# Performance work log

Hardware: AMD Instinct MI355X
Metric: run time of the kernel (lower is better)

The kernel has to match this reference:

```python
import jax, jax.numpy as jnp
import numpy as np

B, H, N, D = 2, 12, 2048, 64
M = int(D * np.log(D))          # 266 performer random features
E3 = 3 * D                      # performer value hidden size = head_dim*3
DH2 = 2 * D                     # predictor enc hidden = head_dim*2
T = 128                         # attention_predictor_length
CHUNK = 128                     # chunk size for causal linear attention scan
KERNEL_EPS = 1e-3               # performer generalized-kernel epsilon
D_EPS = 1e-6                    # denominator epsilon (added to k_cumsum)
LN_EPS = 1e-5


def setup_inputs() -> dict:
    key = jax.random.key(0)
    ks = jax.random.split(key, 10)
    return {
        "q": jax.random.normal(ks[0], (B, H, N, D), jnp.float32),
        "k": jax.random.normal(ks[1], (B, H, N, D), jnp.float32),
        "v3": jax.random.normal(ks[2], (B, H, N, E3), jnp.float32),
        "proj": jax.random.normal(ks[3], (M, D), jnp.float32),
        "enc_w": jax.random.normal(ks[4], (E3, DH2), jnp.float32) * 0.05,
        "enc_b": jnp.zeros((DH2,), jnp.float32),
        "ln_g": jnp.ones((DH2,), jnp.float32),
        "ln_b": jnp.zeros((DH2,), jnp.float32),
        "dec_w": jax.random.normal(ks[5], (DH2, T), jnp.float32) * 0.05,
        "dec_b": jnp.zeros((T,), jnp.float32),
    }


def _generalized_features(x, proj):
    # performer generalized attention kernel: relu((x / d^0.25) @ proj^T) + eps
    dn = 1.0 / (x.shape[-1] ** 0.25)
    xp = jnp.einsum("bhnd,md->bhnm", x * dn, proj)
    return jax.nn.relu(xp) + KERNEL_EPS


def _causal_linear_attention(qf, kf, v):
    # qf, kf: [B,H,N,M]; v: [B,H,N,E]. Chunked recurrent form of
    # out[n] = (qf[n] . cumsum(kf)[n])^-1 * qf[n] @ cumsum(kf[m] v[m]^T)[n]
    nE = v.shape[-1]
    nc = N // CHUNK
    qc = qf.reshape(B, H, nc, CHUNK, M).transpose(2, 0, 1, 3, 4)
    kc = kf.reshape(B, H, nc, CHUNK, M).transpose(2, 0, 1, 3, 4)
    vc = v.reshape(B, H, nc, CHUNK, nE).transpose(2, 0, 1, 3, 4)
    mask = jnp.tril(jnp.ones((CHUNK, CHUNK), qf.dtype))

    def step(carry, inp):
        ksum, S = carry                      # [B,H,M], [B,H,M,E]
        q_c, k_c, v_c = inp                  # [B,H,C,M], [B,H,C,M], [B,H,C,E]
        qk = jnp.einsum("bhim,bhjm->bhij", q_c, k_c) * mask  # causal within chunk
        # denominator: qf[n] . (k_cumsum[n] + eps)
        d = (jnp.einsum("bhcm,bhm->bhc", q_c, ksum)
             + qk.sum(-1)
             + D_EPS * q_c.sum(-1))
        out = (jnp.einsum("bhcm,bhme->bhce", q_c, S)
               + jnp.einsum("bhij,bhje->bhie", qk, v_c)) / d[..., None]
        ksum = ksum + k_c.sum(axis=2)
        S = S + jnp.einsum("bhcm,bhce->bhme", k_c, v_c)
        return (ksum, S), out

    init = (jnp.zeros((B, H, M), qf.dtype), jnp.zeros((B, H, M, nE), qf.dtype))
    _, outs = jax.lax.scan(step, init, (qc, kc, vc))
    return outs.transpose(1, 2, 0, 3, 4).reshape(B, H, N, nE)


def reference(q, k, v3, proj, enc_w, enc_b, ln_g, ln_b, dec_w, dec_b):
    qf = _generalized_features(q, proj)
    kf = _generalized_features(k, proj)
    ctx = _causal_linear_attention(qf, kf, v3)            # [B,H,N,3D]
    # attention predictor: Linear -> LayerNorm -> GELU -> Linear -> softmax
    h = jnp.einsum("bhne,ec->bhnc", ctx, enc_w) + enc_b    # [B,H,N,2D]
    mu = h.mean(-1, keepdims=True)
    var = ((h - mu) ** 2).mean(-1, keepdims=True)
    h = (h - mu) * jax.lax.rsqrt(var + LN_EPS) * ln_g + ln_b
    h = jax.nn.gelu(h, approximate=False)
    scores = jnp.einsum("bhnc,ct->bhnt", h, dec_w) + dec_b  # [B,H,N,T]
    est_probs = jax.nn.softmax(scores, axis=-1)
    return ctx, est_probs
```

## Files before the change

### kernel.cpp

```cpp
#include <hip/hip_runtime.h>
#include <hip/hip_bf16.h>
#include <math.h>

constexpr int Bn = 2, Hn = 12, BHn = 24;
constexpr int Nn = 2048, Dn = 64;
constexpr int Mn = 266, MPn = 272;
constexpr int E3n = 192, DHn = 128, Tn = 128;
constexpr int Cn = 128, NCn = 16;

#define DNRM 0.35355339059327373f
#define KEPS 1e-3f
#define DEPS 1e-6f
#define LNEPS 1e-5f

static const size_t OFF_QF   = 0;
static const size_t OFF_KF   = 26738688;
static const size_t OFF_QK   = 53477376;
static const size_t OFF_D    = 66060288;
static const size_t OFF_KPRE = 66256896;
static const size_t OFF_S    = 66674688;
static const size_t OFF_WT   = OFF_KF;
static const size_t WS_NEED  = 106782720;

using bf16x8 = __attribute__((ext_vector_type(8))) short;
using f32x4  = __attribute__((ext_vector_type(4))) float;

__device__ inline float u2f(unsigned int u) {
  union { float f; unsigned int i; } c; c.i = u << 16; return c.f;
}
__device__ inline unsigned short f2u(float x) {
  __hip_bfloat16 h = __float2bfloat16(x);
  unsigned short u; __builtin_memcpy(&u, &h, 2); return u;
}
__device__ inline void unpack8(uint4 v, float* a) {
  a[0] = u2f(v.x & 0xffffu); a[1] = u2f(v.x >> 16);
  a[2] = u2f(v.y & 0xffffu); a[3] = u2f(v.y >> 16);
  a[4] = u2f(v.z & 0xffffu); a[5] = u2f(v.z >> 16);
  a[6] = u2f(v.w & 0xffffu); a[7] = u2f(v.w >> 16);
}
__device__ inline ushort4 f4tobf(float4 v) {
  ushort4 o;
  o.x = f2u(v.x); o.y = f2u(v.y); o.z = f2u(v.z); o.w = f2u(v.w);
  return o;
}

__global__ __launch_bounds__(256) void k_features_mfma(
    const float* __restrict__ q, const float* __restrict__ k,
    const float* __restrict__ proj,
    unsigned short* __restrict__ qf, unsigned short* __restrict__ kf) {
  __shared__ unsigned short at[64][40];
  __shared__ unsigned short bt[272][40];
  const float* x = (blockIdx.y == 0) ? q : k;
  unsigned short* outp = (blockIdx.y == 0) ? qf : kf;
  int tid = threadIdx.x;
  int w = tid >> 6, l = tid & 63;
  int l16 = l & 15, lg = l >> 4;
  int r0 = blockIdx.x * 64;

  f32x4 acc[17] = {};
  for (int kt = 0; kt < 2; ++kt) {
    int k0 = kt * 32;
    __syncthreads();
    #pragma unroll
    for (int p = 0; p < 2; ++p) {
      int idx = tid + p * 256;
      int row = idx >> 3, kq = idx & 7;
      float4 v = *(const float4*)(x + (size_t)(r0 + row) * Dn + k0 + kq * 4);
      *(ushort4*)&at[row][kq * 4] = f4tobf(v);
    }
    for (int idx = tid; idx < 2176; idx += 256) {
      int mq = idx >> 3, kq = idx & 7;
      float4 v = make_float4(0.f, 0.f, 0.f, 0.f);
      if (mq < Mn) v = *(const float4*)(proj + (size_t)mq * Dn + k0 + kq * 4);
      *(ushort4*)&bt[mq][kq * 4] = f4tobf(v);
    }
    __syncthreads();
    bf16x8 a = *(const bf16x8*)((const char*)&at[0][0] + (w*16 + l16) * 80 + lg * 16);
    #pragma unroll
    for (int ct = 0; ct < 17; ++ct) {
      bf16x8 b = *(const bf16x8*)((const char*)&bt[0][0] + (ct*16 + l16) * 80 + lg * 16);
      acc[ct] = __builtin_amdgcn_mfma_f32_16x16x32_bf16(a, b, acc[ct], 0, 0, 0);
    }
  }
  #pragma unroll
  for (int ct = 0; ct < 17; ++ct)
    #pragma unroll
    for (int reg = 0; reg < 4; ++reg) {
      int row = r0 + w*16 + lg*4 + reg;
      int m = ct*16 + l16;
      float val = 0.f;
      if (m < Mn) val = fmaxf(acc[ct][reg] * DNRM, 0.f) + KEPS;
      outp[(size_t)row * MPn + m] = f2u(val);
    }
}

__global__ __launch_bounds__(256) void k_kprefix(float* __restrict__ kpre) {
  int bh = blockIdx.x; int tid = threadIdx.x;
  for (int m = tid; m < MPn; m += 256) {
    float v[NCn];
    #pragma unroll
    for (int c = 0; c < NCn; ++c) v[c] = kpre[((size_t)bh * NCn + c) * MPn + m];
    float acc = 0.f;
    #pragma unroll
    for (int c = 0; c < NCn; ++c) {
      kpre[((size_t)bh * NCn + c) * MPn + m] = acc;
      acc += v[c];
    }
  }
}

__global__ __launch_bounds__(256) void k_qk_mfma(
    const unsigned short* __restrict__ qf,
    const unsigned short* __restrict__ kf,
    const float* __restrict__ kpre,
    unsigned short* __restrict__ qkout,
    float* __restrict__ dden) {
  __shared__ unsigned short at[128][40];
  __shared__ unsigned short ktl[128][40];
  __shared__ float kp[MPn];
  __shared__ float rs_lds[128];
  int blk = blockIdx.x;
  int bh = blk >> 4, c = blk & 15;
  int tid = threadIdx.x;
  int w = tid >> 6, l = tid & 63;
  int l16 = l & 15, lg = l >> 4;
  size_t qbase = ((size_t)bh * Nn + (size_t)c * Cn) * MPn;
  size_t rbase = (size_t)bh * Nn + (size_t)c * Cn;
  for (int m = tid; m < MPn; m += 256) kp[m] = kpre[((size_t)bh * NCn + c) * MPn + m];

  f32x4 acc[2][8] = {};
  for (int kt = 0; kt < 9; ++kt) {
    int mt = kt * 32;
    __syncthreads();
    #pragma unroll
    for (int p = 0; p < 2; ++p) {
      int idx = tid * 8 + p * 2048;
      int r = idx >> 5, kk = idx & 31;
      uint4 va = make_uint4(0u,0u,0u,0u), vk = make_uint4(0u,0u,0u,0u);
      if (mt + kk < MPn) {
        va = *(const uint4*)(qf + qbase + (size_t)r * MPn + mt + kk);
        vk = *(const uint4*)(kf + qbase + (size_t)r * MPn + mt + kk);
      }
      *(uint4*)((char*)&at[0][0] + r * 80 + kk * 2) = va;
      *(uint4*)((char*)&ktl[0][0] + r * 80 + kk * 2) = vk;
    }
    __syncthreads();
    bf16x8 a0 = *(const bf16x8*)((const char*)&at[0][0] + (w*32 + l16) * 80 + lg * 16);
    bf16x8 a1 = *(const bf16x8*)((const char*)&at[0][0] + (w*32 + 16 + l16) * 80 + lg * 16);
    #pragma unroll
    for (int ct = 0; ct < 8; ++ct) {
      bf16x8 b = *(const bf16x8*)((const char*)&ktl[0][0] + (ct*16 + l16) * 80 + lg * 16);
      acc[0][ct] = __builtin_amdgcn_mfma_f32_16x16x32_bf16(a0, b, acc[0][ct], 0, 0, 0);
      acc[1][ct] = __builtin_amdgcn_mfma_f32_16x16x32_bf16(a1, b, acc[1][ct], 0, 0, 0);
    }
  }
  size_t qkbase = (size_t)blk * (Cn * Cn);
  float rs[2][4] = {};
  #pragma unroll
  for (int rt = 0; rt < 2; ++rt)
    #pragma unroll
    for (int ct = 0; ct < 8; ++ct)
      #pragma unroll
      for (int reg = 0; reg < 4; ++reg) {
        int row = w*32 + rt*16 + lg*4 + reg;
        int col = ct*16 + l16;
        float v = (col <= row) ? acc[rt][ct][reg] : 0.f;
        qkout[qkbase + (size_t)row * Cn + col] = f2u(v);
        rs[rt][reg] += v;
      }
  #pragma unroll
  for (int rt = 0; rt < 2; ++rt)
    #pragma unroll
    for (int reg = 0; reg < 4; ++reg) {
      float s = rs[rt][reg];
      s += __shfl_xor(s, 1); s += __shfl_xor(s, 2);
      s += __shfl_xor(s, 4); s += __shfl_xor(s, 8);
      rs[rt][reg] = s;
    }
  if (l16 == 0) {
    #pragma unroll
    for (int rt = 0; rt < 2; ++rt)
      #pragma unroll
      for (int reg = 0; reg < 4; ++reg)
        rs_lds[w*32 + rt*16 + lg*4 + reg] = rs[rt][reg];
  }
  __syncthreads();
  if (tid < 128) {
    float dot = 0.f, qs = 0.f;
    const unsigned short* qrow = qf + qbase + (size_t)tid * MPn;
    for (int m = 0; m < MPn; m += 8) {
      uint4 v = *(const uint4*)(qrow + m);
      float a[8]; unpack8(v, a);
      #pragma unroll
      for (int t = 0; t < 8; ++t) { dot += a[t] * kp[m + t]; qs += a[t]; }
    }
    dden[rbase + tid] = rs_lds[tid] + dot + DEPS * qs;
  }
}

__global__ __launch_bounds__(768) void k_schunk_mfma(
    const unsigned short* __restrict__ kf,
    const float* __restrict__ v3,
    unsigned short* __restrict__ ST,
    float* __restrict__ kpre) {
  __shared__ unsigned short at[192][40];
  __shared__ unsigned short bt[272][36];
  int blk = blockIdx.x;
  int bh = blk >> 4, c = blk & 15;
  int tid = threadIdx.x;
  int w = tid >> 6, l = tid & 63;
  int l16 = l & 15, lg = l >> 4;
  size_t vbase = ((size_t)bh * Nn + (size_t)c * Cn) * E3n;
  size_t kbase = ((size_t)bh * Nn + (size_t)c * Cn) * MPn;

  f32x4 acc[17] = {};
  float ks = 0.f;
  for (int kt = 0; kt < 4; ++kt) {
    int jt = kt * 32;
    __syncthreads();
    #pragma unroll
    for (int p = 0; p < 2; ++p) {
      int idx = tid + p * 768;
      int j = idx & 31, eq = idx >> 5;
      float4 v = *(const float4*)(v3 + vbase + (size_t)(jt + j) * E3n + eq * 4);
      at[eq*4+0][j] = f2u(v.x); at[eq*4+1][j] = f2u(v.y);
      at[eq*4+2][j] = f2u(v.z); at[eq*4+3][j] = f2u(v.w);
    }
    for (int idx = tid; idx < 1088; idx += 768) {
      int j = idx & 31, mq = idx >> 5;
      uint4 v = *(const uint4*)(kf + kbase + (size_t)(jt + j) * MPn + mq * 8);
      unsigned short tmp[8]; __builtin_memcpy(tmp, &v, 16);
      #pragma unroll
      for (int t = 0; t < 8; ++t) bt[mq*8+t][j] = tmp[t];
    }
    __syncthreads();
    bf16x8 a = *(const bf16x8*)((const char*)&at[0][0] + (w*16 + l16) * 80 + lg * 16);
    #pragma unroll
    for (int ct = 0; ct < 17; ++ct) {
      bf16x8 b = *(const bf16x8*)((const char*)&bt[0][0] + (ct*16 + l16) * 72 + lg * 16);
      acc[ct] = __builtin_amdgcn_mfma_f32_16x16x32_bf16(a, b, acc[ct], 0, 0, 0);
    }
    if (tid < MPn) {
      #pragma unroll
      for (int jq = 0; jq < 4; ++jq) {
        uint4 v = *(const uint4*)((const char*)&bt[0][0] + tid * 72 + jq * 16);
        float a8[8]; unpack8(v, a8);
        #pragma unroll
        for (int t = 0; t < 8; ++t) ks += a8[t];
      }
    }
  }
  size_t stbase = (size_t)blk * MPn * E3n;
  #pragma unroll
  for (int ct = 0; ct < 17; ++ct)
    #pragma unroll
    for (int reg = 0; reg < 4; ++reg) {
      int e_loc = w*16 + lg*4 + reg;
      ST[stbase + (size_t)e_loc * MPn + ct*16 + l16] = f2u(acc[ct][reg]);
    }
  if (tid < MPn)
    kpre[((size_t)bh * NCn + c) * MPn + tid] = ks;
}

__global__ __launch_bounds__(256) void k_wt(const float* __restrict__ enc_w,
    const float* __restrict__ dec_w, unsigned short* __restrict__ ewt,
    unsigned short* __restrict__ dwt) {
  int i = blockIdx.x * 256 + threadIdx.x;
  if (i < 128 * 192) {
    int n = i / 192, e = i - n * 192;
    ewt[i] = f2u(enc_w[(size_t)e * DHn + n]);
  } else {
    int j = i - 128 * 192;
    int t = j >> 7, c = j & 127;
    dwt[(size_t)t * DHn + c] = f2u(dec_w[(size_t)c * Tn + t]);
  }
}

__global__ __launch_bounds__(256) void k_sprefix(unsigned short* __restrict__ S) {
  int bh = blockIdx.x / 51, sub = blockIdx.x % 51;
  int idx4 = sub * 256 + threadIdx.x;
  size_t off = (size_t)idx4 * 4;
  ushort4 v[NCn];
  #pragma unroll
  for (int c = 0; c < NCn; ++c)
    v[c] = *(const ushort4*)(S + ((size_t)(bh * NCn + c)) * MPn * E3n + off);
  float a0 = 0.f, a1 = 0.f, a2 = 0.f, a3 = 0.f;
  #pragma unroll
  for (int c = 0; c < NCn; ++c) {
    ushort4 o;
    unsigned short* op = (unsigned short*)&o;
    op[0] = f2u(a0); op[1] = f2u(a1); op[2] = f2u(a2); op[3] = f2u(a3);
    *(ushort4*)(S + ((size_t)(bh * NCn + c)) * MPn * E3n + off) = o;
    a0 += u2f(v[c].x); a1 += u2f(v[c].y); a2 += u2f(v[c].z); a3 += u2f(v[c].w);
  }
}

__global__ __launch_bounds__(768) void k_ctx_mfma(
    const unsigned short* __restrict__ qf,
    const unsigned short* __restrict__ qkm,
    const unsigned short* __restrict__ ST,
    const float* __restrict__ v3,
    const float* __restrict__ dden,
    float* __restrict__ ctx) {
  __shared__ unsigned short at[128][40];
  __shared__ unsigned short bt[192][40];
  __shared__ float dd[128];
  int blk = blockIdx.x;
  int bh = blk >> 4, c = blk & 15;
  int tid = threadIdx.x;
  int w = tid >> 6, l = tid & 63;
  int l16 = l & 15, lg = l >> 4;
  int wr = w & 3, we = w >> 2;
  size_t qbase = ((size_t)bh * Nn + (size_t)c * Cn) * MPn;
  size_t sbase = (size_t)blk * MPn * E3n;
  size_t rbase = (size_t)bh * Nn + (size_t)c * Cn;
  if (tid < 128) dd[tid] = dden[rbase + tid];

  f32x4 acc[2][4] = {};
  for (int kt = 0; kt < 9; ++kt) {
    int mt = kt * 32;
    __syncthreads();
    if (tid < 512) {
      int r = tid >> 2, kk = (tid & 3) * 8;
      uint4 v = make_uint4(0u,0u,0u,0u);
      if (mt + kk < MPn) v = *(const uint4*)(qf + qbase + (size_t)r * MPn + mt + kk);
      *(uint4*)((char*)&at[0][0] + r * 80 + kk * 2) = v;
    }
    {
      int r = tid >> 2, kk = (tid & 3) * 8;
      uint4 v = make_uint4(0u,0u,0u,0u);
      if (mt + kk < MPn) v = *(const uint4*)(ST + sbase + (size_t)r * MPn + mt + kk);
      *(uint4*)((char*)&bt[0][0] + r * 80 + kk * 2) = v;
    }
    __syncthreads();
    bf16x8 a0 = *(const bf16x8*)((const char*)&at[0][0] + (wr*32 + l16) * 80 + lg * 16);
    bf16x8 a1 = *(const bf16x8*)((const char*)&at[0][0] + (wr*32 + 16 + l16) * 80 + lg * 16);
    #pragma unroll
    for (int ct = 0; ct < 4; ++ct) {
      bf16x8 b = *(const bf16x8*)((const char*)&bt[0][0] + (we*64 + ct*16 + l16) * 80 + lg * 16);
      acc[0][ct] = __builtin_amdgcn_mfma_f32_16x16x32_bf16(a0, b, acc[0][ct], 0, 0, 0);
      acc[1][ct] = __builtin_amdgcn_mfma_f32_16x16x32_bf16(a1, b, acc[1][ct], 0, 0, 0);
    }
  }
  size_t kkbase = (size_t)blk * (Cn * Cn);
  size_t vb3 = ((size_t)bh * Nn + (size_t)c * Cn) * E3n;
  for (int kt = 0; kt < 4; ++kt) {
    int jt = kt * 32;
    __syncthreads();
    if (tid < 512) {
      int r = tid >> 2, kk = (tid & 3) * 8;
      uint4 v = *(const uint4*)(qkm + kkbase + (size_t)r * Cn + jt + kk);
      *(uint4*)((char*)&at[0][0] + r * 80 + kk * 2) = v;
    }
    #pragma unroll
    for (int p = 0; p < 2; ++p) {
      int idx = tid + p * 768;
      int j = idx & 31, eq = idx >> 5;
      float4 v = *(const float4*)(v3 + vb3 + (size_t)(jt + j) * E3n + eq * 4);
      bt[eq*4+0][j] = f2u(v.x); bt[eq*4+1][j] = f2u(v.y);
      bt[eq*4+2][j] = f2u(v.z); bt[eq*4+3][j] = f2u(v.w);
    }
    __syncthreads();
    bf16x8 a0 = *(const bf16x8*)((const char*)&at[0][0] + (wr*32 + l16) * 80 + lg * 16);
    bf16x8 a1 = *(const bf16x8*)((const char*)&at[0][0] + (wr*32 + 16 + l16) * 80 + lg * 16);
    #pragma unroll
    for (int ct = 0; ct < 4; ++ct) {
      bf16x8 b = *(const bf16x8*)((const char*)&bt[0][0] + (we*64 + ct*16 + l16) * 80 + lg * 16);
      acc[0][ct] = __builtin_amdgcn_mfma_f32_16x16x32_bf16(a0, b, acc[0][ct], 0, 0, 0);
      acc[1][ct] = __builtin_amdgcn_mfma_f32_16x16x32_bf16(a1, b, acc[1][ct], 0, 0, 0);
    }
  }
  #pragma unroll
  for (int rt = 0; rt < 2; ++rt)
    #pragma unroll
    for (int ct = 0; ct < 4; ++ct)
      #pragma unroll
      for (int reg = 0; reg < 4; ++reg) {
        int row = wr*32 + rt*16 + lg*4 + reg;
        float inv = 1.f / dd[row];
        ctx[(rbase + row) * (size_t)E3n + we*64 + ct*16 + l16] = acc[rt][ct][reg] * inv;
      }
}

__global__ __launch_bounds__(256) void k_pred_fused(
    const float* __restrict__ ctx,
    const unsigned short* __restrict__ ewt,
    const unsigned short* __restrict__ dwt,
    const float* __restrict__ enc_b, const float* __restrict__ ln_g,
    const float* __restrict__ ln_b, const float* __restrict__ dec_b,
    float* __restrict__ probs) {
  __shared__ unsigned short at[128][40];
  __shared__ unsigned short bt[128][40];
  __shared__ unsigned short ht[128][200];
  int tid = threadIdx.x;
  int w = tid >> 6, l = tid & 63;
  int l16 = l & 15, lg = l >> 4;
  size_t r0 = (size_t)blockIdx.x * 128;

  float ebv[8], ggv[8], llv[8], dbv[8];
  #pragma unroll
  for (int ct = 0; ct < 8; ++ct) {
    ebv[ct] = enc_b[ct*16 + l16];
    ggv[ct] = ln_g[ct*16 + l16];
    llv[ct] = ln_b[ct*16 + l16];
    dbv[ct] = dec_b[ct*16 + l16];
  }

  f32x4 acc1[2][8] = {};
  for (int kt = 0; kt < 6; ++kt) {
    int k0 = kt * 32;
    __syncthreads();
    #pragma unroll
    for (int p = 0; p < 4; ++p) {
      int idx = tid + p * 256;
      int row = idx >> 3, kq = idx & 7;
      float4 v = *(const float4*)(ctx + (r0 + row) * E3n + k0 + kq * 4);
      *(ushort4*)&at[row][kq * 4] = f4tobf(v);
    }
    #pragma unroll
    for (int p = 0; p < 2; ++p) {
      int idx = tid + p * 256;
      int n = idx >> 2, kq = idx & 3;
      *(uint4*)&bt[n][kq * 8] = *(const uint4*)(ewt + (size_t)n * E3n + k0 + kq * 8);
    }
    __syncthreads();
    bf16x8 a0 = *(const bf16x8*)((const char*)&at[0][0] + (w*32 + l16) * 80 + lg * 16);
    bf16x8 a1 = *(const bf16x8*)((const char*)&at[0][0] + (w*32 + 16 + l16) * 80 + lg * 16);
    #pragma unroll
    for (int ct = 0; ct < 8; ++ct) {
      bf16x8 b = *(const bf16x8*)((const char*)&bt[0][0] + (ct*16 + l16) * 80 + lg * 16);
      acc1[0][ct] = __builtin_amdgcn_mfma_f32_16x16x32_bf16(a0, b, acc1[0][ct], 0, 0, 0);
      acc1[1][ct] = __builtin_amdgcn_mfma_f32_16x16x32_bf16(a1, b, acc1[1][ct], 0, 0, 0);
    }
  }
  #pragma unroll
  for (int rt = 0; rt < 2; ++rt) {
    #pragma unroll
    for (int reg = 0; reg < 4; ++reg) {
      float hv[8];
      float s = 0.f, s2 = 0.f;
      #pragma unroll
      for (int ct = 0; ct < 8; ++ct) {
        float v = acc1[rt][ct][reg] + ebv[ct];
        hv[ct] = v; s += v; s2 += v * v;
      }
      #pragma unroll
      for (int m = 1; m < 16; m <<= 1) { s += __shfl_xor(s, m); s2 += __shfl_xor(s2, m); }
      float mu = s * (1.f / 128.f);
      float var = s2 * (1.f / 128.f) - mu * mu;
      float rsq = rsqrtf(var + LNEPS);
      int row = w*32 + rt*16 + lg*4 + reg;
      #pragma unroll
      for (int ct = 0; ct < 8; ++ct) {
        float v = (hv[ct] - mu) * rsq * ggv[ct] + llv[ct];
        v = 0.5f * v * (1.f + erff(v * 0.70710678118654752f));
        ht[row][ct*16 + l16] = f2u(v);
      }
    }
  }
  f32x4 acc2[2][8] = {};
  for (int kt = 0; kt < 4; ++kt) {
    int c0 = kt * 32;
    __syncthreads();
    #pragma unroll
    for (int p = 0; p < 2; ++p) {
      int idx = tid + p * 256;
      int t = idx >> 2, kq = idx & 3;
      *(uint4*)&bt[t][kq * 8] = *(const uint4*)(dwt + (size_t)t * DHn + c0 + kq * 8);
    }
    __syncthreads();
    bf16x8 a0 = *(const bf16x8*)&ht[w*32 + l16][c0 + lg*8];
    bf16x8 a1 = *(const bf16x8*)&ht[w*32 + 16 + l16][c0 + lg*8];
    #pragma unroll
    for (int ct = 0; ct < 8; ++ct) {
      bf16x8 b = *(const bf16x8*)((const char*)&bt[0][0] + (ct*16 + l16) * 80 + lg * 16);
      acc2[0][ct] = __builtin_amdgcn_mfma_f32_16x16x32_bf16(a0, b, acc2[0][ct], 0, 0, 0);
      acc2[1][ct] = __builtin_amdgcn_mfma_f32_16x16x32_bf16(a1, b, acc2[1][ct], 0, 0, 0);
    }
  }
  #pragma unroll
  for (int rt = 0; rt < 2; ++rt) {
    #pragma unroll
    for (int reg = 0; reg < 4; ++reg) {
      float sv[8];
      float m = -1e30f;
      #pragma unroll
      for (int ct = 0; ct < 8; ++ct) {
        sv[ct] = acc2[rt][ct][reg] + dbv[ct];
        m = fmaxf(m, sv[ct]);
      }
      #pragma unroll
      for (int mm = 1; mm < 16; mm <<= 1) m = fmaxf(m, __shfl_xor(m, mm));
      float s = 0.f;
      #pragma unroll
      for (int ct = 0; ct < 8; ++ct) { sv[ct] = expf(sv[ct] - m); s += sv[ct]; }
      #pragma unroll
      for (int mm = 1; mm < 16; mm <<= 1) s += __shfl_xor(s, mm);
      float inv = 1.f / s;
      int row = w*32 + rt*16 + lg*4 + reg;
      #pragma unroll
      for (int ct = 0; ct < 8; ++ct)
        probs[(r0 + row) * (size_t)Tn + ct*16 + l16] = sv[ct] * inv;
    }
  }
}

extern "C" void kernel_launch(void* const* d_in, const int* in_sizes, int n_in,
                              void* d_out, int out_size, void* d_ws, size_t ws_size,
                              hipStream_t stream) {
  const float* q     = (const float*)d_in[0];
  const float* k     = (const float*)d_in[1];
  const float* v3    = (const float*)d_in[2];
  const float* proj  = (const float*)d_in[3];
  const float* enc_w = (const float*)d_in[4];
  const float* enc_b = (const float*)d_in[5];
  const float* ln_g  = (const float*)d_in[6];
  const float* ln_b  = (const float*)d_in[7];
  const float* dec_w = (const float*)d_in[8];
  const float* dec_b = (const float*)d_in[9];
  float* out = (float*)d_out;
  char* ws = (char*)d_ws;
  if (ws_size < WS_NEED) return;

  unsigned short* qf   = (unsigned short*)(ws + OFF_QF);
  unsigned short* kf   = (unsigned short*)(ws + OFF_KF);
  unsigned short* qk   = (unsigned short*)(ws + OFF_QK);
  float*          dden = (float*)(ws + OFF_D);
  float*          kpre = (float*)(ws + OFF_KPRE);
  unsigned short* ST   = (unsigned short*)(ws + OFF_S);
  unsigned short* ewt  = (unsigned short*)(ws + OFF_WT);
  unsigned short* dwt  = (unsigned short*)(ws + OFF_WT + 49152);
  float* ctx   = out;
  float* probs = out + (size_t)BHn * Nn * E3n;

  k_features_mfma<<<dim3(BHn * Nn / 64, 2), 256, 0, stream>>>(q, k, proj, qf, kf);
  k_schunk_mfma <<<dim3(BHn * NCn),     768, 0, stream>>>(kf, v3, ST, kpre);
  k_kprefix     <<<dim3(BHn),           256, 0, stream>>>(kpre);
  k_qk_mfma     <<<dim3(BHn * NCn),     256, 0, stream>>>(qf, kf, kpre, qk, dden);
  k_wt          <<<dim3(160),           256, 0, stream>>>(enc_w, dec_w, ewt, dwt);
  k_sprefix     <<<dim3(BHn * 51),      256, 0, stream>>>(ST);
  k_ctx_mfma    <<<dim3(BHn * NCn),     768, 0, stream>>>(qf, qk, ST, v3, dden, ctx);
  k_pred_fused  <<<dim3(BHn * Nn / 128),256, 0, stream>>>(ctx, ewt, dwt, enc_b, ln_g,
                                                          ln_b, dec_b, probs);
}
```

Measured before the change: 156.9 us.

## Fuse intra-chunk QK^T and denominator computation into the context kernel

Removes the separate k_qk_mfma kernel and computes the masked intra-chunk q·k matrix inside the context kernel, keeping it in shared memory instead of writing and rereading a bf16 global buffer. The denominator is also computed in-kernel and stored as a reciprocal. This saves a launch and the global round trip of the QK and denominator arrays. The cost is more shared memory per block (about 35 KB for the QK tile) and a first phase where only 8 of 12 waves do MFMA work.

```diff
diff --git a/kernel.cpp b/kernel.cpp
--- a/kernel.cpp
+++ b/kernel.cpp
@@ -16,10 +16,9 @@
 static const size_t OFF_QF   = 0;
 static const size_t OFF_KF   = 26738688;
 static const size_t OFF_QK   = 53477376;
-static const size_t OFF_D    = 66060288;
 static const size_t OFF_KPRE = 66256896;
 static const size_t OFF_S    = 66674688;
-static const size_t OFF_WT   = OFF_KF;
+static const size_t OFF_WT   = OFF_QK;
 static const size_t WS_NEED  = 106782720;
 
 using bf16x8 = __attribute__((ext_vector_type(8))) short;
@@ -106,95 +105,6 @@
       kpre[((size_t)bh * NCn + c) * MPn + m] = acc;
       acc += v[c];
     }
-  }
-}
-
-__global__ __launch_bounds__(256) void k_qk_mfma(
-    const unsigned short* __restrict__ qf,
-    const unsigned short* __restrict__ kf,
-    const float* __restrict__ kpre,
-    unsigned short* __restrict__ qkout,
-    float* __restrict__ dden) {
-  __shared__ unsigned short at[128][40];
-  __shared__ unsigned short ktl[128][40];
-  __shared__ float kp[MPn];
-  __shared__ float rs_lds[128];
-  int blk = blockIdx.x;
-  int bh = blk >> 4, c = blk & 15;
-  int tid = threadIdx.x;
-  int w = tid >> 6, l = tid & 63;
-  int l16 = l & 15, lg = l >> 4;
-  size_t qbase = ((size_t)bh * Nn + (size_t)c * Cn) * MPn;
-  size_t rbase = (size_t)bh * Nn + (size_t)c * Cn;
-  for (int m = tid; m < MPn; m += 256) kp[m] = kpre[((size_t)bh * NCn + c) * MPn + m];
-
-  f32x4 acc[2][8] = {};
-  for (int kt = 0; kt < 9; ++kt) {
-    int mt = kt * 32;
-    __syncthreads();
-    #pragma unroll
-    for (int p = 0; p < 2; ++p) {
-      int idx = tid * 8 + p * 2048;
-      int r = idx >> 5, kk = idx & 31;
-      uint4 va = make_uint4(0u,0u,0u,0u), vk = make_uint4(0u,0u,0u,0u);
-      if (mt + kk < MPn) {
-        va = *(const uint4*)(qf + qbase + (size_t)r * MPn + mt + kk);
-        vk = *(const uint4*)(kf + qbase + (size_t)r * MPn + mt + kk);
-      }
-      *(uint4*)((char*)&at[0][0] + r * 80 + kk * 2) = va;
-      *(uint4*)((char*)&ktl[0][0] + r * 80 + kk * 2) = vk;
-    }
-    __syncthreads();
-    bf16x8 a0 = *(const bf16x8*)((const char*)&at[0][0] + (w*32 + l16) * 80 + lg * 16);
-    bf16x8 a1 = *(const bf16x8*)((const char*)&at[0][0] + (w*32 + 16 + l16) * 80 + lg * 16);
-    #pragma unroll
-    for (int ct = 0; ct < 8; ++ct) {
-      bf16x8 b = *(const bf16x8*)((const char*)&ktl[0][0] + (ct*16 + l16) * 80 + lg * 16);
-      acc[0][ct] = __builtin_amdgcn_mfma_f32_16x16x32_bf16(a0, b, acc[0][ct], 0, 0, 0);
-      acc[1][ct] = __builtin_amdgcn_mfma_f32_16x16x32_bf16(a1, b, acc[1][ct], 0, 0, 0);
-    }
-  }
-  size_t qkbase = (size_t)blk * (Cn * Cn);
-  float rs[2][4] = {};
-  #pragma unroll
-  for (int rt = 0; rt < 2; ++rt)
-    #pragma unroll
-    for (int ct = 0; ct < 8; ++ct)
-      #pragma unroll
-      for (int reg = 0; reg < 4; ++reg) {
-        int row = w*32 + rt*16 + lg*4 + reg;
-        int col = ct*16 + l16;
-        float v = (col <= row) ? acc[rt][ct][reg] : 0.f;
-        qkout[qkbase + (size_t)row * Cn + col] = f2u(v);
-        rs[rt][reg] += v;
-      }
-  #pragma unroll
-  for (int rt = 0; rt < 2; ++rt)
-    #pragma unroll
-    for (int reg = 0; reg < 4; ++reg) {
-      float s = rs[rt][reg];
-      s += __shfl_xor(s, 1); s += __shfl_xor(s, 2);
-      s += __shfl_xor(s, 4); s += __shfl_xor(s, 8);
-      rs[rt][reg] = s;
-    }
-  if (l16 == 0) {
-    #pragma unroll
-    for (int rt = 0; rt < 2; ++rt)
-      #pragma unroll
-      for (int reg = 0; reg < 4; ++reg)
-        rs_lds[w*32 + rt*16 + lg*4 + reg] = rs[rt][reg];
-  }
-  __syncthreads();
-  if (tid < 128) {
-    float dot = 0.f, qs = 0.f;
-    const unsigned short* qrow = qf + qbase + (size_t)tid * MPn;
-    for (int m = 0; m < MPn; m += 8) {
-      uint4 v = *(const uint4*)(qrow + m);
-      float a[8]; unpack8(v, a);
-      #pragma unroll
-      for (int t = 0; t < 8; ++t) { dot += a[t] * kp[m + t]; qs += a[t]; }
-    }
-    dden[rbase + tid] = rs_lds[tid] + dot + DEPS * qs;
   }
 }
 
@@ -295,15 +205,18 @@
   }
 }
 
-__global__ __launch_bounds__(768) void k_ctx_mfma(
+__global__ __launch_bounds__(768) void k_attn_mfma(
     const unsigned short* __restrict__ qf,
-    const unsigned short* __restrict__ qkm,
+    const unsigned short* __restrict__ kf,
+    const float* __restrict__ kpre,
     const unsigned short* __restrict__ ST,
     const float* __restrict__ v3,
-    const float* __restrict__ dden,
     float* __restrict__ ctx) {
   __shared__ unsigned short at[128][40];
   __shared__ unsigned short bt[192][40];
+  __shared__ unsigned short qkl[128][136];
+  __shared__ float kp[MPn];
+  __shared__ float rs_lds[128];
   __shared__ float dd[128];
   int blk = blockIdx.x;
   int bh = blk >> 4, c = blk & 15;
@@ -312,11 +225,10 @@
   int l16 = l & 15, lg = l >> 4;
   int wr = w & 3, we = w >> 2;
   size_t qbase = ((size_t)bh * Nn + (size_t)c * Cn) * MPn;
-  size_t sbase = (size_t)blk * MPn * E3n;
   size_t rbase = (size_t)bh * Nn + (size_t)c * Cn;
-  if (tid < 128) dd[tid] = dden[rbase + tid];
-
-  f32x4 acc[2][4] = {};
+  for (int m = tid; m < MPn; m += 768) kp[m] = kpre[((size_t)bh * NCn + c) * MPn + m];
+
+  f32x4 aq[8] = {};
   for (int kt = 0; kt < 9; ++kt) {
     int mt = kt * 32;
     __syncthreads();
@@ -326,6 +238,67 @@
       if (mt + kk < MPn) v = *(const uint4*)(qf + qbase + (size_t)r * MPn + mt + kk);
       *(uint4*)((char*)&at[0][0] + r * 80 + kk * 2) = v;
     }
+    if (tid >= 256) {
+      int t2 = tid - 256;
+      int r = t2 >> 2, kk = (t2 & 3) * 8;
+      uint4 v = make_uint4(0u,0u,0u,0u);
+      if (mt + kk < MPn) v = *(const uint4*)(kf + qbase + (size_t)r * MPn + mt + kk);
+      *(uint4*)((char*)&bt[0][0] + r * 80 + kk * 2) = v;
+    }
+    __syncthreads();
+    if (w < 8) {
+      bf16x8 a = *(const bf16x8*)((const char*)&at[0][0] + (w*16 + l16) * 80 + lg * 16);
+      #pragma unroll
+      for (int ct = 0; ct < 8; ++ct) {
+        bf16x8 b = *(const bf16x8*)((const char*)&bt[0][0] + (ct*16 + l16) * 80 + lg * 16);
+        aq[ct] = __builtin_amdgcn_mfma_f32_16x16x32_bf16(a, b, aq[ct], 0, 0, 0);
+      }
+    }
+  }
+  if (w < 8) {
+    float rs[4] = {};
+    #pragma unroll
+    for (int ct = 0; ct < 8; ++ct)
+      #pragma unroll
+      for (int reg = 0; reg < 4; ++reg) {
+        int row = w*16 + lg*4 + reg;
+        int col = ct*16 + l16;
+        float v = (col <= row) ? aq[ct][reg] : 0.f;
+        qkl[row][col] = f2u(v);
+        rs[reg] += v;
+      }
+    #pragma unroll
+    for (int reg = 0; reg < 4; ++reg) {
+      float s = rs[reg];
+      s += __shfl_xor(s, 1); s += __shfl_xor(s, 2);
+      s += __shfl_xor(s, 4); s += __shfl_xor(s, 8);
+      if (l16 == 0) rs_lds[w*16 + lg*4 + reg] = s;
+    }
+  }
+  __syncthreads();
+  if (tid < 128) {
+    float dot = 0.f, qs = 0.f;
+    const unsigned short* qrow = qf + qbase + (size_t)tid * MPn;
+    for (int m = 0; m < MPn; m += 8) {
+      uint4 v = *(const uint4*)(qrow + m);
+      float a[8]; unpack8(v, a);
+      #pragma unroll
+      for (int t = 0; t < 8; ++t) { dot += a[t] * kp[m + t]; qs += a[t]; }
+    }
+    dd[tid] = 1.f / (rs_lds[tid] + dot + DEPS * qs);
+  }
+
+  f32x4 acc[2][4] = {};
+  size_t sbase = (size_t)blk * MPn * E3n;
+  for (int kt = 0; kt < 9; ++kt) {
+    int mt = kt * 32;
+    __syncthreads();
+    if (tid < 512) {
+      int r = tid >> 2, kk = (tid & 3) * 8;
+      uint4 v = make_uint4(0u,0u,0u,0u);
+      if (mt + kk < MPn) v = *(const uint4*)(qf + qbase + (size_t)r * MPn + mt + kk);
+      *(uint4*)((char*)&at[0][0] + r * 80 + kk * 2) = v;
+    }
     {
       int r = tid >> 2, kk = (tid & 3) * 8;
       uint4 v = make_uint4(0u,0u,0u,0u);
@@ -342,16 +315,10 @@
       acc[1][ct] = __builtin_amdgcn_mfma_f32_16x16x32_bf16(a1, b, acc[1][ct], 0, 0, 0);
     }
   }
-  size_t kkbase = (size_t)blk * (Cn * Cn);
   size_t vb3 = ((size_t)bh * Nn + (size_t)c * Cn) * E3n;
   for (int kt = 0; kt < 4; ++kt) {
     int jt = kt * 32;
     __syncthreads();
-    if (tid < 512) {
-      int r = tid >> 2, kk = (tid & 3) * 8;
-      uint4 v = *(const uint4*)(qkm + kkbase + (size_t)r * Cn + jt + kk);
-      *(uint4*)((char*)&at[0][0] + r * 80 + kk * 2) = v;
-    }
     #pragma unroll
     for (int p = 0; p < 2; ++p) {
       int idx = tid + p * 768;
@@ -361,8 +328,8 @@
       bt[eq*4+2][j] = f2u(v.z); bt[eq*4+3][j] = f2u(v.w);
     }
     __syncthreads();
-    bf16x8 a0 = *(const bf16x8*)((const char*)&at[0][0] + (wr*32 + l16) * 80 + lg * 16);
-    bf16x8 a1 = *(const bf16x8*)((const char*)&at[0][0] + (wr*32 + 16 + l16) * 80 + lg * 16);
+    bf16x8 a0 = *(const bf16x8*)&qkl[wr*32 + l16][jt + lg*8];
+    bf16x8 a1 = *(const bf16x8*)&qkl[wr*32 + 16 + l16][jt + lg*8];
     #pragma unroll
     for (int ct = 0; ct < 4; ++ct) {
       bf16x8 b = *(const bf16x8*)((const char*)&bt[0][0] + (we*64 + ct*16 + l16) * 80 + lg * 16);
@@ -377,8 +344,7 @@
       #pragma unroll
       for (int reg = 0; reg < 4; ++reg) {
         int row = wr*32 + rt*16 + lg*4 + reg;
-        float inv = 1.f / dd[row];
-        ctx[(rbase + row) * (size_t)E3n + we*64 + ct*16 + l16] = acc[rt][ct][reg] * inv;
+        ctx[(rbase + row) * (size_t)E3n + we*64 + ct*16 + l16] = acc[rt][ct][reg] * dd[row];
       }
 }
 
@@ -524,8 +490,6 @@
 
   unsigned short* qf   = (unsigned short*)(ws + OFF_QF);
   unsigned short* kf   = (unsigned short*)(ws + OFF_KF);
-  unsigned short* qk   = (unsigned short*)(ws + OFF_QK);
-  float*          dden = (float*)(ws + OFF_D);
   float*          kpre = (float*)(ws + OFF_KPRE);
   unsigned short* ST   = (unsigned short*)(ws + OFF_S);
   unsigned short* ewt  = (unsigned short*)(ws + OFF_WT);
@@ -536,10 +500,9 @@
   k_features_mfma<<<dim3(BHn * Nn / 64, 2), 256, 0, stream>>>(q, k, proj, qf, kf);
   k_schunk_mfma <<<dim3(BHn * NCn),     768, 0, stream>>>(kf, v3, ST, kpre);
   k_kprefix     <<<dim3(BHn),           256, 0, stream>>>(kpre);
-  k_qk_mfma     <<<dim3(BHn * NCn),     256, 0, stream>>>(qf, kf, kpre, qk, dden);
   k_wt          <<<dim3(160),           256, 0, stream>>>(enc_w, dec_w, ewt, dwt);
   k_sprefix     <<<dim3(BHn * 51),      256, 0, stream>>>(ST);
-  k_ctx_mfma    <<<dim3(BHn * NCn),     768, 0, stream>>>(qf, qk, ST, v3, dden, ctx);
+  k_attn_mfma   <<<dim3(BHn * NCn),     768, 0, stream>>>(qf, kf, kpre, ST, v3, ctx);
   k_pred_fused  <<<dim3(BHn * Nn / 128),256, 0, stream>>>(ctx, ewt, dwt, enc_b, ln_g,
                                                           ln_b, dec_b, probs);
 }
```

After: 171.9 us. +9.5%, slower.
